# Optimization experiments

Hardware: AMD Instinct MI355X
Metric: run time of the kernel (lower is better)

The kernel has to match this reference:

```python
import jax, jax.numpy as jnp
import numpy as np

B, T, N, DIN = 32, 12, 512, 1
H, K, ED, HOR, OD = 64, 3, 10, 12, 1


def setup_inputs() -> dict:
    key = jax.random.key(0)
    ks = jax.random.split(key, 15)
    rn = lambda k, s, sc=0.1: jax.random.normal(k, s, jnp.float32) * sc
    return {
        "source": jax.random.normal(ks[0], (B, T, N, DIN), jnp.float32),
        "targets": jax.random.normal(ks[1], (B, HOR, N, OD), jnp.float32),
        # standard Gumbel(0,1) noise: -log(Exp(1)), matches torch's exponential_().log()
        "gumbel_noise": -jnp.log(jax.random.exponential(ks[2], (N, N, 2), jnp.float32)),
        "emb": jax.random.normal(ks[3], (N, ED), jnp.float32),
        "gw0": rn(ks[4], (ED, K, DIN + H, 2 * H)),
        "gb0": rn(ks[5], (ED, 2 * H)),
        "uw0": rn(ks[6], (ED, K, DIN + H, H)),
        "ub0": rn(ks[7], (ED, H)),
        "gw1": rn(ks[8], (ED, K, 2 * H, 2 * H)),
        "gb1": rn(ks[9], (ED, 2 * H)),
        "uw1": rn(ks[10], (ED, K, 2 * H, H)),
        "ub1": rn(ks[11], (ED, H)),
        "cw": rn(ks[12], (HOR * OD, 1, 1, H)),  # Conv2d(1, HOR*OD, (1, H)) weight
        "cb": rn(ks[13], (HOR * OD,)),
    }


def scaled_laplacian(emb, gnoise):
    sim = emb @ emb.T                                   # [N,N]
    nrm = jnp.linalg.norm(emb, axis=1, keepdims=True)
    lg = sim / (nrm @ nrm.T)
    lg = (lg + 1.0) / 2.0
    logits = jnp.stack([lg, 1.0 - lg], axis=-1)         # [N,N,2]
    # faithful to the pasted gumbel_softmax: y_soft = gumbels (no softmax), tau=1, hard=True
    y_soft = logits + gnoise
    idx = jnp.argmax(y_soft, axis=-1)
    y_hard = jax.nn.one_hot(idx, 2, dtype=logits.dtype)
    ret = y_hard - jax.lax.stop_gradient(y_soft) + y_soft
    adj = ret[:, :, 0] * (1.0 - jnp.eye(N, dtype=logits.dtype))  # zero diagonal
    d = jnp.sum(adj, axis=1)
    L = -adj + jnp.diag(d)                              # diag(adj)=0, so L diag = d
    lam = jnp.max(L) - jnp.min(L)
    tilde = 2.0 * L / lam - jnp.eye(N, dtype=logits.dtype)
    return tilde


def cheb_supports(tilde):
    sup = [jnp.eye(N, dtype=tilde.dtype), tilde]
    for _ in range(2, K):
        sup.append(2.0 * tilde @ sup[-1] - sup[-2])
    return jnp.stack(sup, axis=0)                       # [K,N,N]


def gconv(x, emb, supports, wp, bp):
    # x: [B,N,C]; wp: [ED,K,C,O]; bp: [ED,O]
    xg = jnp.einsum('knm,bmc->bnkc', supports, x)
    w = jnp.einsum('nd,dkio->nkio', emb, wp)
    b = emb @ bp                                        # [N,O]
    return jnp.einsum('bnki,nkio->bno', xg, w) + b


def run_layer(inputs, emb, supports, gw, gb, uw, ub):
    # inputs: [B,T,N,C] -> hidden states [B,T,N,H]
    h0 = jnp.zeros((inputs.shape[0], N, H), inputs.dtype)

    def step(h, x_t):
        xs = jnp.concatenate([x_t, h], axis=-1)
        zr = jax.nn.sigmoid(gconv(xs, emb, supports, gw, gb))
        z, r = zr[..., :H], zr[..., H:]
        cand = jnp.concatenate([x_t, z * h], axis=-1)
        hc = jnp.tanh(gconv(cand, emb, supports, uw, ub))
        h_new = r * h + (1.0 - r) * hc
        return h_new, h_new

    _, hs = jax.lax.scan(step, h0, jnp.swapaxes(inputs, 0, 1))
    return jnp.swapaxes(hs, 0, 1)


def reference(source, targets, gumbel_noise, emb, gw0, gb0, uw0, ub0,
              gw1, gb1, uw1, ub1, cw, cb):
    tilde = scaled_laplacian(emb, gumbel_noise)
    supports = cheb_supports(tilde)
    h1 = run_layer(source, emb, supports, gw0, gb0, uw0, ub0)
    h2 = run_layer(h1, emb, supports, gw1, gb1, uw1, ub1)
    last = h2[:, -1, :, :]                              # [B,N,H]
    # Conv2d(1, HOR*OD, (1,H)) over [B,1,N,H] == per-node linear
    y = jnp.einsum('bnh,oh->bon', last, cw[:, 0, 0, :]) + cb[None, :, None]
    y = y.reshape(-1, HOR, OD, N)
    return jnp.transpose(y, (0, 1, 3, 2))               # [B,HOR,N,OD]
```

## Files before the change

### kernel.cpp

```cpp
#include <hip/hip_runtime.h>
#include <math.h>

#define N_    512
#define B_    32
#define T_    12
#define H_    64
#define ED_   10
#define HOR_  12
#define OUTS_ 4096

typedef unsigned short ushort_t;
typedef __attribute__((ext_vector_type(4))) float f32x4;
typedef __attribute__((ext_vector_type(8))) __bf16 bf16x8;
typedef __attribute__((ext_vector_type(8))) short short8;

__device__ __forceinline__ float sigmoidf_(float x){ return 1.f/(1.f+expf(-x)); }
__device__ __forceinline__ float b2f(ushort_t u){ return __uint_as_float(((unsigned)u)<<16); }
__device__ __forceinline__ ushort_t f2b(float f){
  unsigned x = __float_as_uint(f);
  unsigned r = x + 0x7FFFu + ((x>>16)&1u);
  return (ushort_t)(r>>16);
}
__device__ __forceinline__ void stage16(const void* g, void* l){
  __builtin_amdgcn_global_load_lds(
    (const __attribute__((address_space(1))) unsigned int*)g,
    (__attribute__((address_space(3))) unsigned int*)l, 16, 0, 0);
}

__global__ __launch_bounds__(512) void k_norm(const float* __restrict__ emb, float* __restrict__ nrm){
  int n = threadIdx.x;
  if (n < N_){
    float s = 0.f;
    #pragma unroll
    for (int d=0; d<ED_; ++d){ float v = emb[n*ED_+d]; s += v*v; }
    nrm[n] = sqrtf(s);
  }
}

__global__ __launch_bounds__(256) void k_adj(const float* __restrict__ emb, const float* __restrict__ nrm,
                      const float* __restrict__ gn, ushort_t* __restrict__ Abf, float* __restrict__ dvec){
  __shared__ float ei[ED_];
  __shared__ float red[256];
  int i = blockIdx.x;
  if (threadIdx.x < ED_) ei[threadIdx.x] = emb[i*ED_+threadIdx.x];
  __syncthreads();
  float ni = nrm[i];
  float part = 0.f;
  for (int j = threadIdx.x; j < N_; j += 256){
    float dot = 0.f;
    #pragma unroll
    for (int d=0; d<ED_; ++d) dot += ei[d]*emb[j*ED_+d];
    float lg = (dot/(ni*nrm[j]) + 1.f)*0.5f;
    size_t gi = ((size_t)i*N_ + j)*2;
    float y0 = lg + gn[gi];
    float y1 = (1.f - lg) + gn[gi+1];
    bool a = (j != i && y0 >= y1);
    Abf[(size_t)i*N_ + j] = a ? (ushort_t)0x3F80 : (ushort_t)0;
    part += a ? 1.f : 0.f;
  }
  red[threadIdx.x] = part;
  __syncthreads();
  for (int s=128; s>0; s>>=1){
    if (threadIdx.x < s) red[threadIdx.x] += red[threadIdx.x+s];
    __syncthreads();
  }
  if (threadIdx.x==0) dvec[i] = red[0];
}

__global__ __launch_bounds__(512) void k_lam(const float* __restrict__ dvec, float* __restrict__ lam){
  __shared__ float red[512];
  red[threadIdx.x] = dvec[threadIdx.x];
  __syncthreads();
  for (int s=256; s>0; s>>=1){
    if (threadIdx.x < s) red[threadIdx.x] = fmaxf(red[threadIdx.x], red[threadIdx.x+s]);
    __syncthreads();
  }
  if (threadIdx.x==0){
    float maxd = red[0];
    lam[0] = maxd + (maxd > 0.f ? 1.f : 0.f);
  }
}

__global__ __launch_bounds__(256) void k_a2(const ushort_t* __restrict__ Abf, ushort_t* __restrict__ A2bf){
  __shared__ float ar[N_];
  int n = blockIdx.x;
  for (int p = threadIdx.x; p < N_; p += 256) ar[p] = b2f(Abf[(size_t)n*N_ + p]);
  __syncthreads();
  int m0 = threadIdx.x, m1 = threadIdx.x + 256;
  float a0 = 0.f, a1 = 0.f;
  for (int p=0; p<N_; ++p){
    float ap = ar[p];
    a0 += ap * b2f(Abf[(size_t)p*N_ + m0]);
    a1 += ap * b2f(Abf[(size_t)p*N_ + m1]);
  }
  A2bf[(size_t)n*N_ + m0] = f2b(a0);
  A2bf[(size_t)n*N_ + m1] = f2b(a1);
}

__global__ __launch_bounds__(256) void k_admats(const ushort_t* __restrict__ Abf, const float* __restrict__ dvec,
                        const float* __restrict__ lam, ushort_t* __restrict__ ADh){
  int idx = blockIdx.x*256 + threadIdx.x;
  int m = idx & (N_-1);
  float dm = 2.f*dvec[m]/lam[0] - 1.f;
  ADh[idx] = Abf[idx] ? f2b(dm) : (ushort_t)0;
}

#define TILE_USH 8192
__global__ __launch_bounds__(256) void k_apply(
    const ushort_t* __restrict__ XH, const ushort_t* __restrict__ XL,
    const ushort_t* __restrict__ Abf, const ushort_t* __restrict__ A2bf, const ushort_t* __restrict__ ADh,
    float* __restrict__ P, float* __restrict__ Rm, float* __restrict__ Qm)
{
  __shared__ ushort_t lds[3*TILE_USH];
  const int z = blockIdx.z;
  const ushort_t* M = (z==0)? Abf : (z==1)? A2bf : ADh;
  float* OUT = (z==0)? P : (z==1)? Rm : Qm;
  const int cBase = blockIdx.x<<7, nBase = blockIdx.y<<7;
  const int tid = threadIdx.x, lane = tid&63, w = tid>>6;
  const int wr = w>>1, wc = w&1;
  const int lrow = lane>>3, lslot = lane&7;
  const int srck = lslot ^ (lrow&7);
  const char* g0 = (const char*)XH;
  const char* g1 = (const char*)XL;
  const char* g2 = (const char*)M;
  f32x4 acc[4][4];
  #pragma unroll
  for (int i=0;i<4;++i)
    #pragma unroll
    for (int j=0;j<4;++j) acc[i][j] = f32x4{0.f,0.f,0.f,0.f};
  const int fl = lane&15, kq = lane>>4;

  for (int kk=0; kk<512; kk+=64){
    #pragma unroll
    for (int s=0; s<12; ++s){
      int instId = w + s*4;
      int tile = instId>>4, inst = instId&15;
      const char* g = (tile==0? g0 : (tile==1? g1 : g2));
      int rb = (tile<2? cBase : nBase) + inst*8 + lrow;
      stage16(g + (size_t)rb*(N_*2) + kk*2 + srck*16,
              (char*)lds + tile*16384 + inst*1024);
    }
    __syncthreads();
    #pragma unroll
    for (int kh=0; kh<2; ++kh){
      bf16x8 ah[4], alo[4], bm[4];
      #pragma unroll
      for (int fi=0; fi<4; ++fi){
        int row = (wr<<6) + (fi<<4) + fl;
        int off = (row<<6) + (((kq + (kh<<2)) ^ (row&7))<<3);
        ah[fi]  = *(const bf16x8*)&lds[off];
        alo[fi] = *(const bf16x8*)&lds[TILE_USH + off];
      }
      #pragma unroll
      for (int fj=0; fj<4; ++fj){
        int row = (wc<<6) + (fj<<4) + fl;
        int off = (row<<6) + (((kq + (kh<<2)) ^ (row&7))<<3);
        bm[fj] = *(const bf16x8*)&lds[2*TILE_USH + off];
      }
      #pragma unroll
      for (int fi=0; fi<4; ++fi)
        #pragma unroll
        for (int fj=0; fj<4; ++fj){
          acc[fi][fj] = __builtin_amdgcn_mfma_f32_16x16x32_bf16(ah[fi],  bm[fj], acc[fi][fj], 0,0,0);
          acc[fi][fj] = __builtin_amdgcn_mfma_f32_16x16x32_bf16(alo[fi], bm[fj], acc[fi][fj], 0,0,0);
        }
    }
    __syncthreads();
  }
  #pragma unroll
  for (int fi=0; fi<4; ++fi){
    int cg = cBase + (wr<<6) + (fi<<4) + (kq<<2);
    #pragma unroll
    for (int fj=0; fj<4; ++fj){
      int ng = nBase + (wc<<6) + (fj<<4) + fl;
      float4 v = make_float4(acc[fi][fj][0], acc[fi][fj][1], acc[fi][fj][2], acc[fi][fj][3]);
      *(float4*)&OUT[(size_t)ng*OUTS_ + cg] = v;
    }
  }
}

__global__ __launch_bounds__(256) void k_wmax(const float* __restrict__ wp, const float* __restrict__ emb,
                       unsigned int* __restrict__ sb, int KIO, int O){
  __shared__ float es[N_*ED_];
  for (int e = threadIdx.x; e < N_*ED_; e += 256) es[e] = emb[e];
  __syncthreads();
  int e = blockIdx.x*256 + threadIdx.x;
  if (e >= KIO) return;
  int o = e % O;
  float wv[ED_];
  #pragma unroll
  for (int d=0; d<ED_; ++d) wv[d] = wp[(size_t)d*KIO + e];
  float m = 0.f;
  int n0 = blockIdx.y*64;
  for (int n=n0; n<n0+64; ++n){
    float a = 0.f;
    #pragma unroll
    for (int d=0; d<ED_; ++d) a += es[n*ED_+d]*wv[d];
    m = fmaxf(m, fabsf(a));
  }
  atomicMax(&sb[o], __float_as_uint(m));
}

__global__ __launch_bounds__(256) void k_wquant(const float* __restrict__ wp, const float* __restrict__ emb,
                         const unsigned int* __restrict__ sb, short* __restrict__ W,
                         int KI, int O, int RS){
  __shared__ float es[N_*ED_];
  for (int e = threadIdx.x; e < N_*ED_; e += 256) es[e] = emb[e];
  __syncthreads();
  int KC = RS/8;
  int e = blockIdx.x*256 + threadIdx.x;
  if (e >= KC*O) return;
  int o = e % O, kc = e / O;
  int KIO = KI*O;
  float M = __uint_as_float(sb[o]);
  float inv = (M > 0.f) ? 32767.f/M : 0.f;
  float wv[8][ED_];
  #pragma unroll
  for (int km=0; km<8; ++km){
    int ki = kc*8 + km;
    #pragma unroll
    for (int d=0; d<ED_; ++d)
      wv[km][d] = (ki < KI) ? wp[(size_t)d*KIO + (size_t)ki*O + o] : 0.f;
  }
  int n0 = blockIdx.y*32;
  for (int n=n0; n<n0+32; ++n){
    short8 q;
    #pragma unroll
    for (int km=0; km<8; ++km){
      float a = 0.f;
      #pragma unroll
      for (int d=0; d<ED_; ++d) a += es[n*ED_+d]*wv[km][d];
      q[km] = (short)__float2int_rn(a*inv);
    }
    *(short8*)&W[(((size_t)n*KC + kc)*O + o)*8] = q;
  }
}

__global__ __launch_bounds__(256) void k_bias(const float* __restrict__ bp, const float* __restrict__ emb,
                       float* __restrict__ Bo, int O){
  int idx = blockIdx.x*256 + threadIdx.x;
  int o = idx % O, n = idx / O;
  float a = 0.f;
  #pragma unroll
  for (int d=0; d<ED_; ++d) a += emb[n*ED_+d]*bp[d*O+o];
  Bo[idx] = a;
}

__global__ void k_fill0(float* __restrict__ p, size_t n){
  size_t i = (size_t)blockIdx.x*blockDim.x + threadIdx.x;
  size_t stride = (size_t)gridDim.x*blockDim.x;
  for (; i<n; i+=stride) p[i] = 0.f;
}

__global__ __launch_bounds__(256) void k_btr(const float* __restrict__ S0, const float* __restrict__ S1,
        ushort_t* __restrict__ XH, ushort_t* __restrict__ XL, int CIN, int coff0, int coff1,
        const float* __restrict__ src, int t, int doSrc){
  __shared__ float Tt[64][65];
  const float* S = blockIdx.z ? S1 : S0;
  int coff = blockIdx.z ? coff1 : coff0;
  int mt = blockIdx.x, b = blockIdx.y;
  int r = threadIdx.x >> 6;
  int j = threadIdx.x & 63;
  #pragma unroll
  for (int rr=0; rr<16; ++rr){
    int m = mt*64 + rr*4 + r;
    Tt[rr*4+r][j] = S[((size_t)m*B_ + b)*H_ + j];
  }
  if (doSrc && blockIdx.z==0 && threadIdx.x < 64){
    int m = mt*64 + threadIdx.x;
    float x = src[((size_t)(b*T_+t))*N_ + m];
    size_t o = ((size_t)(b*CIN))*N_ + m;
    ushort_t xh = f2b(x);
    XH[o] = xh; XL[o] = f2b(x - b2f(xh));
  }
  __syncthreads();
  int mr = threadIdx.x & 63;
  int jq = threadIdx.x >> 6;
  #pragma unroll
  for (int jj=0; jj<16; ++jj){
    int jcol = jj*4 + jq;
    float x = Tt[mr][jcol];
    size_t idx = ((size_t)(b*CIN + coff + jcol))*N_ + mt*64 + mr;
    ushort_t xh = f2b(x);
    XH[idx] = xh;
    XL[idx] = f2b(x - b2f(xh));
  }
}

template<int KC, int NBJ, int OSTR, int AS>
__device__ __forceinline__ void contract_i16(const short* __restrict__ Wb,
                                             const float* __restrict__ A0,
                                             float acc[4][NBJ]){
  short8 w0,w1,w2,w3, p0,p1,p2,p3, q0,q1,q2,q3;
  {
    const short8* wp8 = (const short8*)(Wb);
    w0=wp8[0]; w1=wp8[1]; w2=wp8[2]; w3=wp8[3];
    const short8* pp8 = (const short8*)(Wb + OSTR);
    p0=pp8[0]; p1=pp8[1]; p2=pp8[2]; p3=pp8[3];
    q0=p0; q1=p1; q2=p2; q3=p3;
  }
  for (int kc=0; kc<KC; ++kc){
    if (kc+2 < KC){
      const short8* np8 = (const short8*)(Wb + (size_t)(kc+2)*OSTR);
      q0=np8[0]; q1=np8[1]; q2=np8[2]; q3=np8[3];
    }
    #pragma unroll
    for (int kh=0; kh<2; ++kh){
      f32x4 av[NBJ];
      #pragma unroll
      for (int bj=0; bj<NBJ; ++bj) av[bj] = *(const f32x4*)&A0[bj*AS + kc*8 + kh*4];
      #pragma unroll
      for (int u=0; u<4; ++u){
        float f0=(float)w0[kh*4+u], f1=(float)w1[kh*4+u];
        float f2v=(float)w2[kh*4+u], f3=(float)w3[kh*4+u];
        #pragma unroll
        for (int bj=0; bj<NBJ; ++bj){
          acc[0][bj] += av[bj][u]*f0;
          acc[1][bj] += av[bj][u]*f1;
          acc[2][bj] += av[bj][u]*f2v;
          acc[3][bj] += av[bj][u]*f3;
        }
      }
    }
    w0=p0; w1=p1; w2=p2; w3=p3;
    p0=q0; p1=q1; p2=q2; p3=q3;
  }
}

template<int CIN>
__global__ __launch_bounds__(256) void k_gate(
    const float* __restrict__ src, int t,
    const float* __restrict__ hx, const float* __restrict__ hy,
    const float* __restrict__ P, const float* __restrict__ Rm, const float* __restrict__ Qm,
    const float* __restrict__ dvec, const float* __restrict__ lam,
    const short* __restrict__ W, const float* __restrict__ Wsc, const float* __restrict__ Bb,
    const float* __restrict__ hstate,
    float* __restrict__ cand, float* __restrict__ rbuf)
{
  constexpr int O  = 128;
  constexpr int RS = (3*CIN + 7) & ~7;
  constexpr int KC = RS/8;
  constexpr int AS = RS + 4;
  __shared__ float A[B_*AS];
  int n = blockIdx.x;
  float lm = lam[0];
  float al = -2.f/lm;
  float dn = 2.f*dvec[n]/lm - 1.f;
  float c_r = 2.f*al*al, c_q = 2.f*al, c_p = 2.f*al*dn, c_x = 2.f*dn*dn - 1.f;
  for (int e = threadIdx.x; e < B_*CIN; e += 256){
    int b = e/CIN, c = e%CIN;
    float x;
    if (CIN==65) x = (c==0) ? src[((size_t)(b*T_+t))*N_ + n] : hx[(size_t)n*(B_*H_) + b*H_ + (c-1)];
    else         x = (c<H_) ? hx[(size_t)n*(B_*H_) + b*H_ + c] : hy[(size_t)n*(B_*H_) + b*H_ + (c-H_)];
    size_t pi = (size_t)n*OUTS_ + e;
    float pe = P[pi], re = Rm[pi], qe = Qm[pi];
    float* Ab = A + b*AS;
    Ab[c]         = x;
    Ab[CIN+c]     = al*pe + dn*x;
    Ab[2*CIN+c]   = c_r*re + c_q*qe + c_p*pe + c_x*x;
  }
  for (int e = threadIdx.x; e < B_*(AS-3*CIN); e += 256){
    int b = e/(AS-3*CIN), c = e%(AS-3*CIN);
    A[b*AS + 3*CIN + c] = 0.f;
  }
  __syncthreads();
  int ow = threadIdx.x & 31;
  int bq = threadIdx.x >> 5;
  int o0 = ow*4;
  float acc[4][4] = {};
  const short* Wb = W + ((size_t)n*KC*O + o0)*8;
  const float* A0 = A + (bq*4)*AS;
  contract_i16<KC,4,O*8,AS>(Wb, A0, acc);
  #pragma unroll
  for (int oj=0; oj<4; ++oj){
    int o = o0 + oj;
    float sc = Wsc[o]*(1.f/32767.f);
    float bias = Bb[n*O+o];
    if (o < H_){
      #pragma unroll
      for (int bj=0; bj<4; ++bj){
        int b = bq*4 + bj;
        float z = sigmoidf_(acc[oj][bj]*sc + bias);
        size_t hi = (size_t)n*(B_*H_) + b*H_ + o;
        cand[hi] = z*hstate[hi];
      }
    } else {
      int oo = o - H_;
      #pragma unroll
      for (int bj=0; bj<4; ++bj){
        int b = bq*4 + bj;
        rbuf[(size_t)n*(B_*H_) + b*H_ + oo] = sigmoidf_(acc[oj][bj]*sc + bias);
      }
    }
  }
}

template<int CIN>
__global__ __launch_bounds__(256) void k_update(
    const float* __restrict__ src, int t,
    const float* __restrict__ hx, const float* __restrict__ cand,
    const float* __restrict__ P, const float* __restrict__ Rm, const float* __restrict__ Qm,
    const float* __restrict__ dvec, const float* __restrict__ lam,
    const short* __restrict__ W, const float* __restrict__ Wsc, const float* __restrict__ Bb,
    const float* __restrict__ rbuf, float* __restrict__ h)
{
  constexpr int O  = 64;
  constexpr int RS = (3*CIN + 7) & ~7;
  constexpr int KC = RS/8;
  constexpr int AS = RS + 4;
  __shared__ float A[B_*AS];
  int n = blockIdx.x;
  float lm = lam[0];
  float al = -2.f/lm;
  float dn = 2.f*dvec[n]/lm - 1.f;
  float c_r = 2.f*al*al, c_q = 2.f*al, c_p = 2.f*al*dn, c_x = 2.f*dn*dn - 1.f;
  for (int e = threadIdx.x; e < B_*CIN; e += 256){
    int b = e/CIN, c = e%CIN;
    float x;
    if (CIN==65) x = (c==0) ? src[((size_t)(b*T_+t))*N_ + n] : cand[(size_t)n*(B_*H_) + b*H_ + (c-1)];
    else         x = (c<H_) ? hx[(size_t)n*(B_*H_) + b*H_ + c] : cand[(size_t)n*(B_*H_) + b*H_ + (c-H_)];
    size_t pi = (size_t)n*OUTS_ + e;
    float pe = P[pi], re = Rm[pi], qe = Qm[pi];
    float* Ab = A + b*AS;
    Ab[c]         = x;
    Ab[CIN+c]     = al*pe + dn*x;
    Ab[2*CIN+c]   = c_r*re + c_q*qe + c_p*pe + c_x*x;
  }
  for (int e = threadIdx.x; e < B_*(AS-3*CIN); e += 256){
    int b = e/(AS-3*CIN), c = e%(AS-3*CIN);
    A[b*AS + 3*CIN + c] = 0.f;
  }
  __syncthreads();
  int ow = threadIdx.x & 15;
  int bq = threadIdx.x >> 4;
  int o0 = ow*4;
  float acc[4][2] = {};
  const short* Wb = W + ((size_t)n*KC*O + o0)*8;
  const float* A0 = A + (bq*2)*AS;
  contract_i16<KC,2,O*8,AS>(Wb, A0, acc);
  #pragma unroll
  for (int oj=0; oj<4; ++oj){
    int o = o0 + oj;
    float sc = Wsc[o]*(1.f/32767.f);
    float bias = Bb[n*O+o];
    #pragma unroll
    for (int bj=0; bj<2; ++bj){
      int b = bq*2 + bj;
      float hc = tanhf(acc[oj][bj]*sc + bias);
      size_t hidx = (size_t)n*(B_*H_) + b*H_ + o;
      float r = rbuf[hidx];
      h[hidx] = r*h[hidx] + (1.f-r)*hc;
    }
  }
}

__global__ __launch_bounds__(256) void k_readout(const float* __restrict__ hB, const float* __restrict__ cw,
                          const float* __restrict__ cb, float* __restrict__ out){
  int idx = blockIdx.x*256 + threadIdx.x;
  int n = idx & (N_-1);
  int bo = idx >> 9;
  int o = bo % HOR_, b = bo / HOR_;
  float a = cb[o];
  #pragma unroll
  for (int j=0;j<H_;++j) a += hB[(size_t)n*(B_*H_) + b*H_ + j]*cw[o*H_+j];
  out[idx] = a;
}

extern "C" void kernel_launch(void* const* d_in, const int* in_sizes, int n_in,
                              void* d_out, int out_size, void* d_ws, size_t ws_size,
                              hipStream_t stream){
  (void)in_sizes; (void)n_in; (void)out_size; (void)ws_size;
  const float* src  = (const float*)d_in[0];
  const float* gn   = (const float*)d_in[2];
  const float* emb  = (const float*)d_in[3];
  const float* gw0  = (const float*)d_in[4];
  const float* gb0  = (const float*)d_in[5];
  const float* uw0  = (const float*)d_in[6];
  const float* ub0  = (const float*)d_in[7];
  const float* gw1  = (const float*)d_in[8];
  const float* gb1  = (const float*)d_in[9];
  const float* uw1  = (const float*)d_in[10];
  const float* ub1  = (const float*)d_in[11];
  const float* cw   = (const float*)d_in[12];
  const float* cb   = (const float*)d_in[13];
  float* out = (float*)d_out;

  const int RS0 = 200;
  const int RS1 = 384;

  char* ws = (char*)d_ws;
  size_t off = 0;
  auto alloc = [&](size_t bytes)->char*{
    char* p = ws + off; off = (off + bytes + 255) & ~(size_t)255; return p;
  };
  short* Wg0 = (short*)alloc((size_t)N_*128*RS0*2);
  short* Wu0 = (short*)alloc((size_t)N_*64*RS0*2);
  short* Wg1 = (short*)alloc((size_t)N_*128*RS1*2);
  short* Wu1 = (short*)alloc((size_t)N_*64*RS1*2);
  unsigned int* Sg0 = (unsigned int*)alloc(128*4);
  unsigned int* Su0 = (unsigned int*)alloc(64*4);
  unsigned int* Sg1 = (unsigned int*)alloc(128*4);
  unsigned int* Su1 = (unsigned int*)alloc(64*4);
  float* Bg0 = (float*)alloc((size_t)N_*128*4);
  float* Bu0 = (float*)alloc((size_t)N_*64*4);
  float* Bg1 = (float*)alloc((size_t)N_*128*4);
  float* Bu1 = (float*)alloc((size_t)N_*64*4);
  ushort_t* Abf  = (ushort_t*)alloc((size_t)N_*N_*2);
  ushort_t* A2bf = (ushort_t*)alloc((size_t)N_*N_*2);
  ushort_t* ADh  = (ushort_t*)alloc((size_t)N_*N_*2);
  float* dvec = (float*)alloc(N_*4);
  float* lam  = (float*)alloc(256);
  float* nrm  = (float*)alloc(N_*4);
  float* hA   = (float*)alloc((size_t)N_*B_*H_*4);
  float* hB   = (float*)alloc((size_t)N_*B_*H_*4);
  float* rbuf = (float*)alloc((size_t)N_*B_*H_*4);
  float* cand = (float*)alloc((size_t)N_*B_*H_*4);
  ushort_t* XH = (ushort_t*)alloc((size_t)4096*N_*2);
  ushort_t* XL = (ushort_t*)alloc((size_t)4096*N_*2);
  float* P  = (float*)alloc((size_t)N_*OUTS_*4);
  float* R  = (float*)alloc((size_t)N_*OUTS_*4);
  float* Q  = (float*)alloc((size_t)N_*OUTS_*4);

  const float* fSg0 = (const float*)Sg0;
  const float* fSu0 = (const float*)Su0;
  const float* fSg1 = (const float*)Sg1;
  const float* fSu1 = (const float*)Su1;

  k_norm<<<1,512,0,stream>>>(emb, nrm);
  k_adj<<<N_,256,0,stream>>>(emb, nrm, gn, Abf, dvec);
  k_lam<<<1,512,0,stream>>>(dvec, lam);
  k_a2<<<N_,256,0,stream>>>(Abf, A2bf);
  k_admats<<<(N_*N_)/256,256,0,stream>>>(Abf, dvec, lam, ADh);

  k_fill0<<<1,256,0,stream>>>((float*)Sg0, 384);
  k_wmax<<<dim3((195*128+255)/256,8),256,0,stream>>>(gw0, emb, Sg0, 195*128, 128);
  k_wmax<<<dim3((195*64+255)/256,8),256,0,stream>>>(uw0, emb, Su0, 195*64, 64);
  k_wmax<<<dim3((384*128)/256,8),256,0,stream>>>(gw1, emb, Sg1, 384*128, 128);
  k_wmax<<<dim3((384*64)/256,8),256,0,stream>>>(uw1, emb, Su1, 384*64, 64);
  k_wquant<<<dim3((25*128+255)/256,16),256,0,stream>>>(gw0, emb, Sg0, Wg0, 195, 128, RS0);
  k_wquant<<<dim3((25*64+255)/256,16),256,0,stream>>>(uw0, emb, Su0, Wu0, 195, 64, RS0);
  k_wquant<<<dim3((48*128)/256,16),256,0,stream>>>(gw1, emb, Sg1, Wg1, 384, 128, RS1);
  k_wquant<<<dim3((48*64)/256,16),256,0,stream>>>(uw1, emb, Su1, Wu1, 384, 64, RS1);
  k_bias<<<(N_*128)/256,256,0,stream>>>(gb0, emb, Bg0, 128);
  k_bias<<<(N_*64)/256,256,0,stream>>>(ub0, emb, Bu0, 64);
  k_bias<<<(N_*128)/256,256,0,stream>>>(gb1, emb, Bg1, 128);
  k_bias<<<(N_*64)/256,256,0,stream>>>(ub1, emb, Bu1, 64);

  k_fill0<<<2048,256,0,stream>>>(hA, (size_t)N_*B_*H_);
  k_fill0<<<2048,256,0,stream>>>(hB, (size_t)N_*B_*H_);

  for (int t=0; t<T_; ++t){
    k_btr<<<dim3(8,32,1),256,0,stream>>>(hA, hA, XH, XL, 65, 1, 1, src, t, 1);
    k_apply<<<dim3(17,4,3),256,0,stream>>>(XH, XL, Abf, A2bf, ADh, P, R, Q);
    k_gate<65><<<N_,256,0,stream>>>(src, t, hA, hA, P, R, Q, dvec, lam,
                                    Wg0, fSg0, Bg0, hA, cand, rbuf);
    k_btr<<<dim3(8,32,1),256,0,stream>>>(cand, cand, XH, XL, 65, 1, 1, nullptr, 0, 0);
    k_apply<<<dim3(17,4,3),256,0,stream>>>(XH, XL, Abf, A2bf, ADh, P, R, Q);
    k_update<65><<<N_,256,0,stream>>>(src, t, hA, cand, P, R, Q, dvec, lam,
                                      Wu0, fSu0, Bu0, rbuf, hA);
    k_btr<<<dim3(8,32,2),256,0,stream>>>(hA, hB, XH, XL, 128, 0, 64, nullptr, 0, 0);
    k_apply<<<dim3(32,4,3),256,0,stream>>>(XH, XL, Abf, A2bf, ADh, P, R, Q);
    k_gate<128><<<N_,256,0,stream>>>(nullptr, 0, hA, hB, P, R, Q, dvec, lam,
                                     Wg1, fSg1, Bg1, hB, cand, rbuf);
    k_btr<<<dim3(8,32,1),256,0,stream>>>(cand, cand, XH, XL, 128, 64, 64, nullptr, 0, 0);
    k_apply<<<dim3(32,4,3),256,0,stream>>>(XH, XL, Abf, A2bf, ADh, P, R, Q);
    k_update<128><<<N_,256,0,stream>>>(nullptr, 0, hA, cand, P, R, Q, dvec, lam,
                                       Wu1, fSu1, Bu1, rbuf, hB);
  }

  k_readout<<<(B_*HOR_*N_)/256,256,0,stream>>>(hB, cw, cb, out);
}
```

Before: 2.946 ms.

## Halve k_apply node tile to double grid; restructure k_wmax with in-block reduction

k_apply now computes 128x64 output tiles instead of 128x128, with each wave owning 32 rows across all 64 columns. This doubles the grid in y and shrinks LDS use, aiming to fill more compute units on the small propagation GEMMs. The cost is more re-reading of the X tiles from global memory. k_wmax is also reworked so each thread loops over several input rows and 128 nodes, then reduces in shared memory before issuing one atomicMax per output, which cuts the number of atomics.

```diff
diff --git a/kernel.cpp b/kernel.cpp
--- a/kernel.cpp
+++ b/kernel.cpp
@@ -105,34 +105,33 @@
   ADh[idx] = Abf[idx] ? f2b(dm) : (ushort_t)0;
 }
 
-#define TILE_USH 8192
+#define XTILE_USH 8192
 __global__ __launch_bounds__(256) void k_apply(
     const ushort_t* __restrict__ XH, const ushort_t* __restrict__ XL,
     const ushort_t* __restrict__ Abf, const ushort_t* __restrict__ A2bf, const ushort_t* __restrict__ ADh,
     float* __restrict__ P, float* __restrict__ Rm, float* __restrict__ Qm)
 {
-  __shared__ ushort_t lds[3*TILE_USH];
+  __shared__ ushort_t lds[2*XTILE_USH + 4096];
   const int z = blockIdx.z;
   const ushort_t* M = (z==0)? Abf : (z==1)? A2bf : ADh;
   float* OUT = (z==0)? P : (z==1)? Rm : Qm;
-  const int cBase = blockIdx.x<<7, nBase = blockIdx.y<<7;
+  const int cBase = blockIdx.x<<7, nBase = blockIdx.y<<6;
   const int tid = threadIdx.x, lane = tid&63, w = tid>>6;
-  const int wr = w>>1, wc = w&1;
   const int lrow = lane>>3, lslot = lane&7;
   const int srck = lslot ^ (lrow&7);
   const char* g0 = (const char*)XH;
   const char* g1 = (const char*)XL;
   const char* g2 = (const char*)M;
-  f32x4 acc[4][4];
-  #pragma unroll
-  for (int i=0;i<4;++i)
+  f32x4 acc[2][4];
+  #pragma unroll
+  for (int i=0;i<2;++i)
     #pragma unroll
     for (int j=0;j<4;++j) acc[i][j] = f32x4{0.f,0.f,0.f,0.f};
   const int fl = lane&15, kq = lane>>4;
 
   for (int kk=0; kk<512; kk+=64){
     #pragma unroll
-    for (int s=0; s<12; ++s){
+    for (int s=0; s<10; ++s){
       int instId = w + s*4;
       int tile = instId>>4, inst = instId&15;
       const char* g = (tile==0? g0 : (tile==1? g1 : g2));
@@ -143,22 +142,22 @@
     __syncthreads();
     #pragma unroll
     for (int kh=0; kh<2; ++kh){
-      bf16x8 ah[4], alo[4], bm[4];
-      #pragma unroll
-      for (int fi=0; fi<4; ++fi){
-        int row = (wr<<6) + (fi<<4) + fl;
+      bf16x8 ah[2], alo[2], bm[4];
+      #pragma unroll
+      for (int fi=0; fi<2; ++fi){
+        int row = (w<<5) + (fi<<4) + fl;
         int off = (row<<6) + (((kq + (kh<<2)) ^ (row&7))<<3);
         ah[fi]  = *(const bf16x8*)&lds[off];
-        alo[fi] = *(const bf16x8*)&lds[TILE_USH + off];
+        alo[fi] = *(const bf16x8*)&lds[XTILE_USH + off];
       }
       #pragma unroll
       for (int fj=0; fj<4; ++fj){
-        int row = (wc<<6) + (fj<<4) + fl;
+        int row = (fj<<4) + fl;
         int off = (row<<6) + (((kq + (kh<<2)) ^ (row&7))<<3);
-        bm[fj] = *(const bf16x8*)&lds[2*TILE_USH + off];
+        bm[fj] = *(const bf16x8*)&lds[2*XTILE_USH + off];
       }
       #pragma unroll
-      for (int fi=0; fi<4; ++fi)
+      for (int fi=0; fi<2; ++fi)
         #pragma unroll
         for (int fj=0; fj<4; ++fj){
           acc[fi][fj] = __builtin_amdgcn_mfma_f32_16x16x32_bf16(ah[fi],  bm[fj], acc[fi][fj], 0,0,0);
@@ -168,11 +167,11 @@
     __syncthreads();
   }
   #pragma unroll
-  for (int fi=0; fi<4; ++fi){
-    int cg = cBase + (wr<<6) + (fi<<4) + (kq<<2);
+  for (int fi=0; fi<2; ++fi){
+    int cg = cBase + (w<<5) + (fi<<4) + (kq<<2);
     #pragma unroll
     for (int fj=0; fj<4; ++fj){
-      int ng = nBase + (wc<<6) + (fj<<4) + fl;
+      int ng = nBase + (fj<<4) + fl;
       float4 v = make_float4(acc[fi][fj][0], acc[fi][fj][1], acc[fi][fj][2], acc[fi][fj][3]);
       *(float4*)&OUT[(size_t)ng*OUTS_ + cg] = v;
     }
@@ -180,25 +179,36 @@
 }
 
 __global__ __launch_bounds__(256) void k_wmax(const float* __restrict__ wp, const float* __restrict__ emb,
-                       unsigned int* __restrict__ sb, int KIO, int O){
+                       unsigned int* __restrict__ sb, int KI, int O, int KB){
   __shared__ float es[N_*ED_];
+  __shared__ float sm[256];
   for (int e = threadIdx.x; e < N_*ED_; e += 256) es[e] = emb[e];
   __syncthreads();
-  int e = blockIdx.x*256 + threadIdx.x;
-  if (e >= KIO) return;
-  int o = e % O;
-  float wv[ED_];
-  #pragma unroll
-  for (int d=0; d<ED_; ++d) wv[d] = wp[(size_t)d*KIO + e];
+  int G = 256/O;
+  int o = threadIdx.x % O;
+  int g = threadIdx.x / O;
+  int KIend = min(KI, (int)(blockIdx.x+1)*KB);
+  int n0 = blockIdx.y*128;
+  size_t KIO = (size_t)KI*O;
   float m = 0.f;
-  int n0 = blockIdx.y*64;
-  for (int n=n0; n<n0+64; ++n){
-    float a = 0.f;
-    #pragma unroll
-    for (int d=0; d<ED_; ++d) a += es[n*ED_+d]*wv[d];
-    m = fmaxf(m, fabsf(a));
-  }
-  atomicMax(&sb[o], __float_as_uint(m));
+  for (int ki = blockIdx.x*KB + g; ki < KIend; ki += G){
+    float wv[ED_];
+    #pragma unroll
+    for (int d=0; d<ED_; ++d) wv[d] = wp[(size_t)d*KIO + (size_t)ki*O + o];
+    for (int n=n0; n<n0+128; ++n){
+      float a = 0.f;
+      #pragma unroll
+      for (int d=0; d<ED_; ++d) a += es[n*ED_+d]*wv[d];
+      m = fmaxf(m, fabsf(a));
+    }
+  }
+  sm[threadIdx.x] = m;
+  __syncthreads();
+  for (int s=128; s>=O; s>>=1){
+    if (threadIdx.x < s) sm[threadIdx.x] = fmaxf(sm[threadIdx.x], sm[threadIdx.x+s]);
+    __syncthreads();
+  }
+  if (threadIdx.x < O) atomicMax(&sb[o], __float_as_uint(sm[threadIdx.x]));
 }
 
 __global__ __launch_bounds__(256) void k_wquant(const float* __restrict__ wp, const float* __restrict__ emb,
@@ -533,10 +543,10 @@
   k_admats<<<(N_*N_)/256,256,0,stream>>>(Abf, dvec, lam, ADh);
 
   k_fill0<<<1,256,0,stream>>>((float*)Sg0, 384);
-  k_wmax<<<dim3((195*128+255)/256,8),256,0,stream>>>(gw0, emb, Sg0, 195*128, 128);
-  k_wmax<<<dim3((195*64+255)/256,8),256,0,stream>>>(uw0, emb, Su0, 195*64, 64);
-  k_wmax<<<dim3((384*128)/256,8),256,0,stream>>>(gw1, emb, Sg1, 384*128, 128);
-  k_wmax<<<dim3((384*64)/256,8),256,0,stream>>>(uw1, emb, Su1, 384*64, 64);
+  k_wmax<<<dim3(17,4),256,0,stream>>>(gw0, emb, Sg0, 195, 128, 12);
+  k_wmax<<<dim3(13,4),256,0,stream>>>(uw0, emb, Su0, 195, 64, 16);
+  k_wmax<<<dim3(32,4),256,0,stream>>>(gw1, emb, Sg1, 384, 128, 12);
+  k_wmax<<<dim3(24,4),256,0,stream>>>(uw1, emb, Su1, 384, 64, 16);
   k_wquant<<<dim3((25*128+255)/256,16),256,0,stream>>>(gw0, emb, Sg0, Wg0, 195, 128, RS0);
   k_wquant<<<dim3((25*64+255)/256,16),256,0,stream>>>(uw0, emb, Su0, Wu0, 195, 64, RS0);
   k_wquant<<<dim3((48*128)/256,16),256,0,stream>>>(gw1, emb, Sg1, Wg1, 384, 128, RS1);
@@ -551,19 +561,19 @@
 
   for (int t=0; t<T_; ++t){
     k_btr<<<dim3(8,32,1),256,0,stream>>>(hA, hA, XH, XL, 65, 1, 1, src, t, 1);
-    k_apply<<<dim3(17,4,3),256,0,stream>>>(XH, XL, Abf, A2bf, ADh, P, R, Q);
+    k_apply<<<dim3(17,8,3),256,0,stream>>>(XH, XL, Abf, A2bf, ADh, P, R, Q);
     k_gate<65><<<N_,256,0,stream>>>(src, t, hA, hA, P, R, Q, dvec, lam,
                                     Wg0, fSg0, Bg0, hA, cand, rbuf);
     k_btr<<<dim3(8,32,1),256,0,stream>>>(cand, cand, XH, XL, 65, 1, 1, nullptr, 0, 0);
-    k_apply<<<dim3(17,4,3),256,0,stream>>>(XH, XL, Abf, A2bf, ADh, P, R, Q);
+    k_apply<<<dim3(17,8,3),256,0,stream>>>(XH, XL, Abf, A2bf, ADh, P, R, Q);
     k_update<65><<<N_,256,0,stream>>>(src, t, hA, cand, P, R, Q, dvec, lam,
                                       Wu0, fSu0, Bu0, rbuf, hA);
     k_btr<<<dim3(8,32,2),256,0,stream>>>(hA, hB, XH, XL, 128, 0, 64, nullptr, 0, 0);
-    k_apply<<<dim3(32,4,3),256,0,stream>>>(XH, XL, Abf, A2bf, ADh, P, R, Q);
+    k_apply<<<dim3(32,8,3),256,0,stream>>>(XH, XL, Abf, A2bf, ADh, P, R, Q);
     k_gate<128><<<N_,256,0,stream>>>(nullptr, 0, hA, hB, P, R, Q, dvec, lam,
                                      Wg1, fSg1, Bg1, hB, cand, rbuf);
     k_btr<<<dim3(8,32,1),256,0,stream>>>(cand, cand, XH, XL, 128, 64, 64, nullptr, 0, 0);
-    k_apply<<<dim3(32,4,3),256,0,stream>>>(XH, XL, Abf, A2bf, ADh, P, R, Q);
+    k_apply<<<dim3(32,8,3),256,0,stream>>>(XH, XL, Abf, A2bf, ADh, P, R, Q);
     k_update<128><<<N_,256,0,stream>>>(nullptr, 0, hA, cand, P, R, Q, dvec, lam,
                                        Wu1, fSu1, Bu1, rbuf, hB);
   }
```

Result: no change. 2.929 ms (-0.6%).
